# Kernel optimization log

Hardware: AMD Instinct MI355X
Metric: run time of the kernel (lower is better)

## Reference

```python
import jax, jax.numpy as jnp
import numpy as np

NUM_HEADS = 4

def setup_inputs() -> dict:
    key = jax.random.key(0)
    ks = jax.random.split(key, 9)
    C = 256
    def w(k, shape, scale):
        return jax.random.normal(k, shape, dtype=jnp.float32) * scale
    s = 1.0 / np.sqrt(C)
    return {
        'x':  w(ks[0], (1, C, 48, 48), 1.0),
        'Wq': w(ks[1], (C, C), s), 'bq': w(ks[2], (C,), 0.01),
        'Wk': w(ks[3], (C, C), s), 'bk': w(ks[4], (C,), 0.01),
        'Wv': w(ks[5], (C, C), s), 'bv': w(ks[6], (C,), 0.01),
        'Wo': w(ks[7], (C, C), s), 'bo': w(ks[8], (C,), 0.01),
    }

def reference(x, Wq, bq, Wk, bk, Wv, bv, Wo, bo):
    # x: [B, C, H, W] (NCHW like torch). 1x1 convs == per-pixel matmuls in NHWC.
    B, C, H, W = x.shape
    nh = NUM_HEADS
    xt = jnp.transpose(x, (0, 2, 3, 1))                 # [B,H,W,C]
    q = xt @ Wq.T + bq                                  # [B,H,W,Ck]
    k = xt @ Wk.T + bk                                  # [B,H,W,Ck]
    v = xt @ Wv.T + bv                                  # [B,H,W,Cv]
    dk = q.shape[-1] // nh
    dv = v.shape[-1] // nh
    # split heads then FULLY flatten (batch*H*W*heads), as in the original
    qf = q.reshape(B * H * W * nh, dk) / jnp.sqrt(jnp.float32(dk))
    kf = k.reshape(B * H * W * nh, dk)
    vf = v.reshape(B * H * W * nh, dv)
    A = jax.nn.softmax(qf @ kf.T, axis=1)               # [N,N], N = B*H*W*nh
    # dropout is identity in eval mode
    O = A @ vf                                          # [N,dv]
    O = O.reshape(B, H, W, nh * dv)                     # heads folded back into channels
    out = O @ Wo.T + bo                                 # 1x1 output conv
    return jnp.transpose(out, (0, 3, 1, 2))             # [B,Cout,H,W]
```

## Files before the change

### kernel.cpp

```cpp
#include <hip/hip_runtime.h>
#include <stdint.h>

typedef __attribute__((ext_vector_type(4))) float f32x4;
typedef __attribute__((ext_vector_type(8))) short bf16x8;

#define MFMA(a, b, c) __builtin_amdgcn_mfma_f32_16x16x32_bf16(a, b, c, 0, 0, 0)

__device__ __forceinline__ short f2b(float f) {
    uint32_t u = __builtin_bit_cast(uint32_t, f);
    u += 0x7fffu + ((u >> 16) & 1u);
    return (short)(u >> 16);
}

__device__ __forceinline__ float ex2(float x) {
    float r; asm("v_exp_f32 %0, %1" : "=v"(r) : "v"(x)); return r;
}
__device__ __forceinline__ float ex2c(float x) { return ex2(fminf(x, 60.0f)); }
__device__ __forceinline__ uint32_t cvtpk(float lo, float hi) {
    uint32_t r; asm("v_cvt_pk_bf16_f32 %0, %1, %2" : "=v"(r) : "v"(lo), "v"(hi)); return r;
}
__device__ __forceinline__ float lo2f(uint32_t u) {
    return __builtin_bit_cast(float, (uint32_t)(u << 16));
}
__device__ __forceinline__ float hi2f(uint32_t u) {
    return __builtin_bit_cast(float, (uint32_t)(u & 0xffff0000u));
}

typedef __attribute__((address_space(1))) const uint32_t gu32;
typedef __attribute__((address_space(3))) uint32_t su32;
__device__ __forceinline__ void stage16(const void* g, void* s) {
    __builtin_amdgcn_global_load_lds((gu32*)g, (su32*)s, 16, 0, 0);
}

__device__ __forceinline__ int FSW(int r) { return (r & 3) | (((r >> 3) & 1) << 2); }

#define QSCALE 0.1803368801111601f

__global__ __launch_bounds__(256) void kp_16(
    const float* __restrict__ x,
    const float* __restrict__ Wq, const float* __restrict__ Wk,
    const float* __restrict__ Wv, const float* __restrict__ Wo,
    short* __restrict__ Wall, short* __restrict__ xt) {
    __shared__ float tile[64][65];
    if (blockIdx.x < 1024) {
        int idx = blockIdx.x * 256 + threadIdx.x;
        int row = idx >> 8, col = idx & 255;
        float v;
        if (row < 256)      v = Wq[row * 256 + col];
        else if (row < 512) v = Wk[(row - 256) * 256 + col];
        else if (row < 768) v = Wv[(row - 512) * 256 + col];
        else                v = Wo[(row - 768) * 256 + col];
        Wall[idx] = f2b(v);
    } else {
        int b = blockIdx.x - 1024;
        int pbase = (b % 36) * 64, cbase = (b / 36) * 64;
        int tx = threadIdx.x & 63, tq = threadIdx.x >> 6;
        #pragma unroll
        for (int r = 0; r < 16; r++) {
            int row = tq * 16 + r;
            tile[row][tx] = x[(cbase + row) * 2304 + pbase + tx];
        }
        __syncthreads();
        #pragma unroll
        for (int r = 0; r < 16; r++) {
            int prow = tq * 16 + r;
            xt[(pbase + prow) * 256 + cbase + tx] = f2b(tile[tx][prow]);
        }
    }
}

__global__ __launch_bounds__(256) void kqkv_16(
    const short* __restrict__ Wall, const short* __restrict__ xt,
    const float* __restrict__ bq, const float* __restrict__ bk, const float* __restrict__ bv,
    short* __restrict__ Qf, short* __restrict__ Kf, short* __restrict__ Vt) {
    int t = threadIdx.x, wave = t >> 6, lane = t & 63, lr = lane & 15, lg = lane >> 4;
    int obase = blockIdx.x * 64 + wave * 16;
    int pbase = blockIdx.y * 64;
    const short* arow  = Wall + (obase + lr) * 256 + lg * 8;
    const short* brow0 = xt + (pbase +  0 + lr) * 256 + lg * 8;
    const short* brow1 = xt + (pbase + 16 + lr) * 256 + lg * 8;
    const short* brow2 = xt + (pbase + 32 + lr) * 256 + lg * 8;
    const short* brow3 = xt + (pbase + 48 + lr) * 256 + lg * 8;
    f32x4 acc0 = {0,0,0,0}, acc1 = {0,0,0,0}, acc2 = {0,0,0,0}, acc3 = {0,0,0,0};
    #pragma unroll
    for (int ks = 0; ks < 8; ks++) {
        bf16x8 a = *(const bf16x8*)(arow + ks * 32);
        acc0 = MFMA(a, *(const bf16x8*)(brow0 + ks * 32), acc0);
        acc1 = MFMA(a, *(const bf16x8*)(brow1 + ks * 32), acc1);
        acc2 = MFMA(a, *(const bf16x8*)(brow2 + ks * 32), acc2);
        acc3 = MFMA(a, *(const bf16x8*)(brow3 + ks * 32), acc3);
    }
    int w_idx = obase >> 8;
    const float* bias = (w_idx == 0) ? bq : (w_idx == 1) ? bk : bv;
    f32x4 accs[4] = {acc0, acc1, acc2, acc3};
    #pragma unroll
    for (int i = 0; i < 4; i++) {
        int o = obase + 4 * lg + i;
        int oo = o & 255;
        float b = bias[oo];
        int h = oo >> 6, d = oo & 63;
        #pragma unroll
        for (int ct = 0; ct < 4; ct++) {
            int p = pbase + ct * 16 + lr;
            float val = accs[ct][i] + b;
            int n = p * 4 + h;
            if (w_idx == 0)      Qf[n * 64 + d] = f2b(val * QSCALE);
            else if (w_idx == 1) Kf[n * 64 + d] = f2b(val);
            else                 Vt[d * 9216 + n] = f2b(val);
        }
    }
}

__global__ __launch_bounds__(256) void kat_16(
    const short* __restrict__ Qf, const short* __restrict__ Kf,
    const short* __restrict__ Vt, int keysPer, int ntiles,
    float* __restrict__ ps, uint32_t* __restrict__ pacc) {
    __shared__ short ktile[2][4096];
    __shared__ short vtile[2][4096];
    int t = threadIdx.x, wave = t >> 6, lane = t & 63, lr = lane & 15, lg = lane >> 4;
    int kb = blockIdx.y;
    int qbase = blockIdx.x * 128 + wave * 16;
    int kstart = kb * keysPer;

    const short* qrowA = Qf + (qbase + lr) * 64 + lg * 8;
    bf16x8 qA0 = *(const bf16x8*)(qrowA);
    bf16x8 qA1 = *(const bf16x8*)(qrowA + 32);
    const short* qrowB = qrowA + 64 * 64;
    bf16x8 qB0 = *(const bf16x8*)(qrowB);
    bf16x8 qB1 = *(const bf16x8*)(qrowB + 32);

    bf16x8 ones;
    #pragma unroll
    for (int i = 0; i < 8; i++) ones[i] = (short)0x3F80;

    int sr = lane >> 3, slot = lane & 7;
    int srow0 = wave * 16 + sr, srow1 = srow0 + 8;
    int col0 = (slot ^ FSW(srow0)) << 4;
    int col1 = (slot ^ FSW(srow1)) << 4;
    const char* kS0 = (const char*)Kf + (size_t)(kstart + srow0) * 128 + col0;
    const char* kS1 = (const char*)Kf + (size_t)(kstart + srow1) * 128 + col1;
    const char* vS0 = (const char*)Vt + (size_t)srow0 * 18432 + (size_t)kstart * 2 + col0;
    const char* vS1 = (const char*)Vt + (size_t)srow1 * 18432 + (size_t)kstart * 2 + col1;
    short* kD0[2] = { &ktile[0][wave * 1024], &ktile[1][wave * 1024] };
    short* kD1[2] = { kD0[0] + 512, kD0[1] + 512 };
    short* vD0[2] = { &vtile[0][wave * 1024], &vtile[1][wave * 1024] };
    short* vD1[2] = { vD0[0] + 512, vD0[1] + 512 };

    int perm = (lr & 3) + 8 * (lr >> 2);
    int cb = lg * 16;
    int kOffA0 = perm * 128       + (cb        ^ (FSW(perm) << 4));
    int kOffA1 = perm * 128       + ((cb + 64) ^ (FSW(perm) << 4));
    int kOffB0 = (perm + 4) * 128 + (cb        ^ (FSW(perm + 4) << 4));
    int kOffB1 = (perm + 4) * 128 + ((cb + 64) ^ (FSW(perm + 4) << 4));
    int vOff   = lr * 128         + (cb        ^ (FSW(lr) << 4));

    f32x4 zv = {0,0,0,0};
    f32x4 accA0 = zv, accA1 = zv, accA2 = zv, accA3 = zv, saccA = zv;
    f32x4 accB0 = zv, accB1 = zv, accB2 = zv, accB3 = zv, saccB = zv;

    stage16(kS0, kD0[0]); stage16(kS1, kD1[0]);
    stage16(vS0, vD0[0]); stage16(vS1, vD1[0]);

    for (int tt = 0; tt < ntiles; tt++) {
        __syncthreads();
        int buf = tt & 1;
        if (tt + 1 < ntiles) {
            size_t ko = (size_t)(tt + 1) * 8192, vo = (size_t)(tt + 1) * 128;
            stage16(kS0 + ko, kD0[buf ^ 1]); stage16(kS1 + ko, kD1[buf ^ 1]);
            stage16(vS0 + vo, vD0[buf ^ 1]); stage16(vS1 + vo, vD1[buf ^ 1]);
        }
        const char* kt = (const char*)&ktile[buf][0];
        const char* vt = (const char*)&vtile[buf][0];

        bf16x8 kA0 = *(const bf16x8*)(kt + kOffA0);
        bf16x8 kA1 = *(const bf16x8*)(kt + kOffA1);
        bf16x8 kB0 = *(const bf16x8*)(kt + kOffB0);
        bf16x8 kB1 = *(const bf16x8*)(kt + kOffB1);
        f32x4 sA0 = MFMA(kA0, qA0, zv); sA0 = MFMA(kA1, qA1, sA0);
        f32x4 sA1 = MFMA(kB0, qA0, zv); sA1 = MFMA(kB1, qA1, sA1);
        f32x4 sB0 = MFMA(kA0, qB0, zv); sB0 = MFMA(kA1, qB1, sB0);
        f32x4 sB1 = MFMA(kB0, qB0, zv); sB1 = MFMA(kB1, qB1, sB1);
        kA0 = *(const bf16x8*)(kt + 4096 + kOffA0);
        kA1 = *(const bf16x8*)(kt + 4096 + kOffA1);
        kB0 = *(const bf16x8*)(kt + 4096 + kOffB0);
        kB1 = *(const bf16x8*)(kt + 4096 + kOffB1);
        f32x4 sA2 = MFMA(kA0, qA0, zv); sA2 = MFMA(kA1, qA1, sA2);
        f32x4 sA3 = MFMA(kB0, qA0, zv); sA3 = MFMA(kB1, qA1, sA3);
        f32x4 sB2 = MFMA(kA0, qB0, zv); sB2 = MFMA(kA1, qB1, sB2);
        f32x4 sB3 = MFMA(kB0, qB0, zv); sB3 = MFMA(kB1, qB1, sB3);

        union { uint32_t w[4]; bf16x8 v; } paA, pbA, paB, pbB;
        paA.w[0] = cvtpk(ex2c(sA0[0]), ex2c(sA0[1]));
        paA.w[1] = cvtpk(ex2c(sA0[2]), ex2c(sA0[3]));
        paA.w[2] = cvtpk(ex2c(sA1[0]), ex2c(sA1[1]));
        paA.w[3] = cvtpk(ex2c(sA1[2]), ex2c(sA1[3]));
        pbA.w[0] = cvtpk(ex2c(sA2[0]), ex2c(sA2[1]));
        pbA.w[1] = cvtpk(ex2c(sA2[2]), ex2c(sA2[3]));
        pbA.w[2] = cvtpk(ex2c(sA3[0]), ex2c(sA3[1]));
        pbA.w[3] = cvtpk(ex2c(sA3[2]), ex2c(sA3[3]));
        paB.w[0] = cvtpk(ex2c(sB0[0]), ex2c(sB0[1]));
        paB.w[1] = cvtpk(ex2c(sB0[2]), ex2c(sB0[3]));
        paB.w[2] = cvtpk(ex2c(sB1[0]), ex2c(sB1[1]));
        paB.w[3] = cvtpk(ex2c(sB1[2]), ex2c(sB1[3]));
        pbB.w[0] = cvtpk(ex2c(sB2[0]), ex2c(sB2[1]));
        pbB.w[1] = cvtpk(ex2c(sB2[2]), ex2c(sB2[3]));
        pbB.w[2] = cvtpk(ex2c(sB3[0]), ex2c(sB3[1]));
        pbB.w[3] = cvtpk(ex2c(sB3[2]), ex2c(sB3[3]));

        bf16x8 v0a = *(const bf16x8*)(vt + vOff);
        bf16x8 v0b = *(const bf16x8*)(vt + (vOff ^ 64));
        bf16x8 v1a = *(const bf16x8*)(vt + vOff + 2048);
        bf16x8 v1b = *(const bf16x8*)(vt + ((vOff + 2048) ^ 64));
        bf16x8 v2a = *(const bf16x8*)(vt + vOff + 4096);
        bf16x8 v2b = *(const bf16x8*)(vt + ((vOff + 4096) ^ 64));
        bf16x8 v3a = *(const bf16x8*)(vt + vOff + 6144);
        bf16x8 v3b = *(const bf16x8*)(vt + ((vOff + 6144) ^ 64));
        accA0 = MFMA(v0a, paA.v, accA0); accA0 = MFMA(v0b, pbA.v, accA0);
        accA1 = MFMA(v1a, paA.v, accA1); accA1 = MFMA(v1b, pbA.v, accA1);
        accA2 = MFMA(v2a, paA.v, accA2); accA2 = MFMA(v2b, pbA.v, accA2);
        accA3 = MFMA(v3a, paA.v, accA3); accA3 = MFMA(v3b, pbA.v, accA3);
        saccA = MFMA(ones, paA.v, saccA); saccA = MFMA(ones, pbA.v, saccA);
        accB0 = MFMA(v0a, paB.v, accB0); accB0 = MFMA(v0b, pbB.v, accB0);
        accB1 = MFMA(v1a, paB.v, accB1); accB1 = MFMA(v1b, pbB.v, accB1);
        accB2 = MFMA(v2a, paB.v, accB2); accB2 = MFMA(v2b, pbB.v, accB2);
        accB3 = MFMA(v3a, paB.v, accB3); accB3 = MFMA(v3b, pbB.v, accB3);
        saccB = MFMA(ones, paB.v, saccB); saccB = MFMA(ones, pbB.v, saccB);
    }

    int gA = blockIdx.x * 8 + wave;
    int gB = gA + 4;
    int pidxA = kb * 576 + gA, pidxB = kb * 576 + gB;
    uint2* outA = (uint2*)pacc + (size_t)pidxA * 256 + lr * 16 + lg;
    uint2* outB = (uint2*)pacc + (size_t)pidxB * 256 + lr * 16 + lg;
    uint2 w;
    w.x = cvtpk(accA0[0], accA0[1]); w.y = cvtpk(accA0[2], accA0[3]); outA[0]  = w;
    w.x = cvtpk(accA1[0], accA1[1]); w.y = cvtpk(accA1[2], accA1[3]); outA[4]  = w;
    w.x = cvtpk(accA2[0], accA2[1]); w.y = cvtpk(accA2[2], accA2[3]); outA[8]  = w;
    w.x = cvtpk(accA3[0], accA3[1]); w.y = cvtpk(accA3[2], accA3[3]); outA[12] = w;
    w.x = cvtpk(accB0[0], accB0[1]); w.y = cvtpk(accB0[2], accB0[3]); outB[0]  = w;
    w.x = cvtpk(accB1[0], accB1[1]); w.y = cvtpk(accB1[2], accB1[3]); outB[4]  = w;
    w.x = cvtpk(accB2[0], accB2[1]); w.y = cvtpk(accB2[2], accB2[3]); outB[8]  = w;
    w.x = cvtpk(accB3[0], accB3[1]); w.y = cvtpk(accB3[2], accB3[3]); outB[12] = w;
    if (lg == 0) {
        ps[pidxA * 16 + lr] = saccA[0];
        ps[pidxB * 16 + lr] = saccB[0];
    }
}

__global__ __launch_bounds__(256) void kcmb_16(
    const float* __restrict__ ps, const uint32_t* __restrict__ pacc,
    short* __restrict__ Of, int nsplit) {
    int qb = blockIdx.x, t = threadIdx.x;
    int q = t >> 4, dv4 = (t & 15) * 4;
    float S = 0.f;
    f32x4 O = {0, 0, 0, 0};
    for (int s = 0; s < nsplit; s++) {
        S += ps[(s * 576 + qb) * 16 + q];
        uint2 v = ((const uint2*)pacc)[(size_t)(s * 576 + qb) * 256 + t];
        O[0] += lo2f(v.x); O[1] += hi2f(v.x);
        O[2] += lo2f(v.y); O[3] += hi2f(v.y);
    }
    float inv = 1.0f / fmaxf(S, 1e-30f);
    uint32_t w0 = cvtpk(O[0] * inv, O[1] * inv);
    uint32_t w1 = cvtpk(O[2] * inv, O[3] * inv);
    int n = qb * 16 + q, p = n >> 2, hh = n & 3;
    uint2 pk; pk.x = w0; pk.y = w1;
    *(uint2*)(&Of[p * 256 + hh * 64 + dv4]) = pk;
}

__global__ __launch_bounds__(256) void kout_16(
    const short* __restrict__ Wo_bf, const short* __restrict__ Of,
    const float* __restrict__ bo, float* __restrict__ out) {
    int t = threadIdx.x, wave = t >> 6, lane = t & 63, lr = lane & 15, lg = lane >> 4;
    int obase = blockIdx.x * 64 + wave * 16;
    int pbase = blockIdx.y * 64;
    const short* arow  = Wo_bf + (obase + lr) * 256 + lg * 8;
    const short* brow0 = Of + (pbase +  0 + lr) * 256 + lg * 8;
    const short* brow1 = Of + (pbase + 16 + lr) * 256 + lg * 8;
    const short* brow2 = Of + (pbase + 32 + lr) * 256 + lg * 8;
    const short* brow3 = Of + (pbase + 48 + lr) * 256 + lg * 8;
    f32x4 acc0 = {0,0,0,0}, acc1 = {0,0,0,0}, acc2 = {0,0,0,0}, acc3 = {0,0,0,0};
    #pragma unroll
    for (int ks = 0; ks < 8; ks++) {
        bf16x8 a = *(const bf16x8*)(arow + ks * 32);
        acc0 = MFMA(a, *(const bf16x8*)(brow0 + ks * 32), acc0);
        acc1 = MFMA(a, *(const bf16x8*)(brow1 + ks * 32), acc1);
        acc2 = MFMA(a, *(const bf16x8*)(brow2 + ks * 32), acc2);
        acc3 = MFMA(a, *(const bf16x8*)(brow3 + ks * 32), acc3);
    }
    f32x4 accs[4] = {acc0, acc1, acc2, acc3};
    #pragma unroll
    for (int i = 0; i < 4; i++) {
        int o = obase + 4 * lg + i;
        float b = bo[o];
        #pragma unroll
        for (int ct = 0; ct < 4; ct++) {
            int p = pbase + ct * 16 + lr;
            out[o * 2304 + p] = accs[ct][i] + b;
        }
    }
}

extern "C" void kernel_launch(void* const* d_in, const int* in_sizes, int n_in,
                              void* d_out, int out_size, void* d_ws, size_t ws_size,
                              hipStream_t stream) {
    const float* x  = (const float*)d_in[0];
    const float* Wq = (const float*)d_in[1];
    const float* bq = (const float*)d_in[2];
    const float* Wk = (const float*)d_in[3];
    const float* bk = (const float*)d_in[4];
    const float* Wv = (const float*)d_in[5];
    const float* bv = (const float*)d_in[6];
    const float* Wo = (const float*)d_in[7];
    const float* bo = (const float*)d_in[8];

    char* ws = (char*)d_ws;
    short* Wall = (short*)(ws);
    short* xt   = (short*)(ws + 524288);
    short* Qf   = (short*)(ws + 1703936);
    short* Kf   = (short*)(ws + 2883584);
    short* Vt   = (short*)(ws + 4063232);
    short* Of   = (short*)(ws + 5242880);
    float* ps   = (float*)(ws + 6422528);
    uint32_t* pacc = (uint32_t*)(ws + 7012352);
    float* out  = (float*)d_out;

    size_t base = 7012352;
    int nsplit = (ws_size >= base + 16u * 576u * 2048u) ? 16
               : (ws_size >= base +  8u * 576u * 2048u) ? 8 : 4;
    int keysPer = 9216 / nsplit;
    int ntiles = keysPer / 64;

    kp_16<<<1168, 256, 0, stream>>>(x, Wq, Wk, Wv, Wo, Wall, xt);
    kqkv_16<<<dim3(12, 36), 256, 0, stream>>>(Wall, xt, bq, bk, bv, Qf, Kf, Vt);
    kat_16<<<dim3(72, nsplit), 256, 0, stream>>>(Qf, Kf, Vt, keysPer, ntiles, ps, pacc);
    kcmb_16<<<576, 256, 0, stream>>>(ps, pacc, Of, nsplit);
    kout_16<<<dim3(4, 36), 256, 0, stream>>>(Wall + 768 * 256, Of, bo, out);
}
```

Baseline: 71.37 us.

## Halve attention queries per block and reduce key split count

The attention kernel now handles 64 queries per block (one 16-row group per wave) instead of 128, so each K/V tile staged in LDS is reused by half as many queries. The grid doubles along the query axis. The maximum key split drops from 16 to 8, which gives each block more key tiles and less partial data for the combine kernel to read. Register pressure falls and occupancy may rise, but K/V traffic from global memory into LDS doubles for each query.

Result: no change. 72.62 us (+1.8%).

```diff
diff --git a/kernel.cpp b/kernel.cpp
--- a/kernel.cpp
+++ b/kernel.cpp
@@ -36,7 +36,7 @@
 
 #define QSCALE 0.1803368801111601f
 
-__global__ __launch_bounds__(256) void kp_16(
+__global__ __launch_bounds__(256) void kp_17(
     const float* __restrict__ x,
     const float* __restrict__ Wq, const float* __restrict__ Wk,
     const float* __restrict__ Wv, const float* __restrict__ Wo,
@@ -69,7 +69,7 @@
     }
 }
 
-__global__ __launch_bounds__(256) void kqkv_16(
+__global__ __launch_bounds__(256) void kqkv_17(
     const short* __restrict__ Wall, const short* __restrict__ xt,
     const float* __restrict__ bq, const float* __restrict__ bk, const float* __restrict__ bv,
     short* __restrict__ Qf, short* __restrict__ Kf, short* __restrict__ Vt) {
@@ -111,7 +111,7 @@
     }
 }
 
-__global__ __launch_bounds__(256) void kat_16(
+__global__ __launch_bounds__(256) void kat_17(
     const short* __restrict__ Qf, const short* __restrict__ Kf,
     const short* __restrict__ Vt, int keysPer, int ntiles,
     float* __restrict__ ps, uint32_t* __restrict__ pacc) {
@@ -119,15 +119,12 @@
     __shared__ short vtile[2][4096];
     int t = threadIdx.x, wave = t >> 6, lane = t & 63, lr = lane & 15, lg = lane >> 4;
     int kb = blockIdx.y;
-    int qbase = blockIdx.x * 128 + wave * 16;
+    int qbase = blockIdx.x * 64 + wave * 16;
     int kstart = kb * keysPer;
 
-    const short* qrowA = Qf + (qbase + lr) * 64 + lg * 8;
-    bf16x8 qA0 = *(const bf16x8*)(qrowA);
-    bf16x8 qA1 = *(const bf16x8*)(qrowA + 32);
-    const short* qrowB = qrowA + 64 * 64;
-    bf16x8 qB0 = *(const bf16x8*)(qrowB);
-    bf16x8 qB1 = *(const bf16x8*)(qrowB + 32);
+    const short* qrow = Qf + (qbase + lr) * 64 + lg * 8;
+    bf16x8 q0 = *(const bf16x8*)(qrow);
+    bf16x8 q1 = *(const bf16x8*)(qrow + 32);
 
     bf16x8 ones;
     #pragma unroll
@@ -155,8 +152,7 @@
     int vOff   = lr * 128         + (cb        ^ (FSW(lr) << 4));
 
     f32x4 zv = {0,0,0,0};
-    f32x4 accA0 = zv, accA1 = zv, accA2 = zv, accA3 = zv, saccA = zv;
-    f32x4 accB0 = zv, accB1 = zv, accB2 = zv, accB3 = zv, saccB = zv;
+    f32x4 acc0 = zv, acc1 = zv, acc2 = zv, acc3 = zv, sacc = zv;
 
     stage16(kS0, kD0[0]); stage16(kS1, kD1[0]);
     stage16(vS0, vD0[0]); stage16(vS1, vD1[0]);
@@ -176,36 +172,24 @@
         bf16x8 kA1 = *(const bf16x8*)(kt + kOffA1);
         bf16x8 kB0 = *(const bf16x8*)(kt + kOffB0);
         bf16x8 kB1 = *(const bf16x8*)(kt + kOffB1);
-        f32x4 sA0 = MFMA(kA0, qA0, zv); sA0 = MFMA(kA1, qA1, sA0);
-        f32x4 sA1 = MFMA(kB0, qA0, zv); sA1 = MFMA(kB1, qA1, sA1);
-        f32x4 sB0 = MFMA(kA0, qB0, zv); sB0 = MFMA(kA1, qB1, sB0);
-        f32x4 sB1 = MFMA(kB0, qB0, zv); sB1 = MFMA(kB1, qB1, sB1);
+        f32x4 s0 = MFMA(kA0, q0, zv); s0 = MFMA(kA1, q1, s0);
+        f32x4 s1 = MFMA(kB0, q0, zv); s1 = MFMA(kB1, q1, s1);
         kA0 = *(const bf16x8*)(kt + 4096 + kOffA0);
         kA1 = *(const bf16x8*)(kt + 4096 + kOffA1);
         kB0 = *(const bf16x8*)(kt + 4096 + kOffB0);
         kB1 = *(const bf16x8*)(kt + 4096 + kOffB1);
-        f32x4 sA2 = MFMA(kA0, qA0, zv); sA2 = MFMA(kA1, qA1, sA2);
-        f32x4 sA3 = MFMA(kB0, qA0, zv); sA3 = MFMA(kB1, qA1, sA3);
-        f32x4 sB2 = MFMA(kA0, qB0, zv); sB2 = MFMA(kA1, qB1, sB2);
-        f32x4 sB3 = MFMA(kB0, qB0, zv); sB3 = MFMA(kB1, qB1, sB3);
-
-        union { uint32_t w[4]; bf16x8 v; } paA, pbA, paB, pbB;
-        paA.w[0] = cvtpk(ex2c(sA0[0]), ex2c(sA0[1]));
-        paA.w[1] = cvtpk(ex2c(sA0[2]), ex2c(sA0[3]));
-        paA.w[2] = cvtpk(ex2c(sA1[0]), ex2c(sA1[1]));
-        paA.w[3] = cvtpk(ex2c(sA1[2]), ex2c(sA1[3]));
-        pbA.w[0] = cvtpk(ex2c(sA2[0]), ex2c(sA2[1]));
-        pbA.w[1] = cvtpk(ex2c(sA2[2]), ex2c(sA2[3]));
-        pbA.w[2] = cvtpk(ex2c(sA3[0]), ex2c(sA3[1]));
-        pbA.w[3] = cvtpk(ex2c(sA3[2]), ex2c(sA3[3]));
-        paB.w[0] = cvtpk(ex2c(sB0[0]), ex2c(sB0[1]));
-        paB.w[1] = cvtpk(ex2c(sB0[2]), ex2c(sB0[3]));
-        paB.w[2] = cvtpk(ex2c(sB1[0]), ex2c(sB1[1]));
-        paB.w[3] = cvtpk(ex2c(sB1[2]), ex2c(sB1[3]));
-        pbB.w[0] = cvtpk(ex2c(sB2[0]), ex2c(sB2[1]));
-        pbB.w[1] = cvtpk(ex2c(sB2[2]), ex2c(sB2[3]));
-        pbB.w[2] = cvtpk(ex2c(sB3[0]), ex2c(sB3[1]));
-        pbB.w[3] = cvtpk(ex2c(sB3[2]), ex2c(sB3[3]));
+        f32x4 s2 = MFMA(kA0, q0, zv); s2 = MFMA(kA1, q1, s2);
+        f32x4 s3 = MFMA(kB0, q0, zv); s3 = MFMA(kB1, q1, s3);
+
+        union { uint32_t w[4]; bf16x8 v; } pa, pb;
+        pa.w[0] = cvtpk(ex2c(s0[0]), ex2c(s0[1]));
+        pa.w[1] = cvtpk(ex2c(s0[2]), ex2c(s0[3]));
+        pa.w[2] = cvtpk(ex2c(s1[0]), ex2c(s1[1]));
+        pa.w[3] = cvtpk(ex2c(s1[2]), ex2c(s1[3]));
+        pb.w[0] = cvtpk(ex2c(s2[0]), ex2c(s2[1]));
+        pb.w[1] = cvtpk(ex2c(s2[2]), ex2c(s2[3]));
+        pb.w[2] = cvtpk(ex2c(s3[0]), ex2c(s3[1]));
+        pb.w[3] = cvtpk(ex2c(s3[2]), ex2c(s3[3]));
 
         bf16x8 v0a = *(const bf16x8*)(vt + vOff);
         bf16x8 v0b = *(const bf16x8*)(vt + (vOff ^ 64));
@@ -215,39 +199,27 @@
         bf16x8 v2b = *(const bf16x8*)(vt + ((vOff + 4096) ^ 64));
         bf16x8 v3a = *(const bf16x8*)(vt + vOff + 6144);
         bf16x8 v3b = *(const bf16x8*)(vt + ((vOff + 6144) ^ 64));
-        accA0 = MFMA(v0a, paA.v, accA0); accA0 = MFMA(v0b, pbA.v, accA0);
-        accA1 = MFMA(v1a, paA.v, accA1); accA1 = MFMA(v1b, pbA.v, accA1);
-        accA2 = MFMA(v2a, paA.v, accA2); accA2 = MFMA(v2b, pbA.v, accA2);
-        accA3 = MFMA(v3a, paA.v, accA3); accA3 = MFMA(v3b, pbA.v, accA3);
-        saccA = MFMA(ones, paA.v, saccA); saccA = MFMA(ones, pbA.v, saccA);
-        accB0 = MFMA(v0a, paB.v, accB0); accB0 = MFMA(v0b, pbB.v, accB0);
-        accB1 = MFMA(v1a, paB.v, accB1); accB1 = MFMA(v1b, pbB.v, accB1);
-        accB2 = MFMA(v2a, paB.v, accB2); accB2 = MFMA(v2b, pbB.v, accB2);
-        accB3 = MFMA(v3a, paB.v, accB3); accB3 = MFMA(v3b, pbB.v, accB3);
-        saccB = MFMA(ones, paB.v, saccB); saccB = MFMA(ones, pbB.v, saccB);
-    }
-
-    int gA = blockIdx.x * 8 + wave;
-    int gB = gA + 4;
-    int pidxA = kb * 576 + gA, pidxB = kb * 576 + gB;
-    uint2* outA = (uint2*)pacc + (size_t)pidxA * 256 + lr * 16 + lg;
-    uint2* outB = (uint2*)pacc + (size_t)pidxB * 256 + lr * 16 + lg;
+        acc0 = MFMA(v0a, pa.v, acc0); acc0 = MFMA(v0b, pb.v, acc0);
+        acc1 = MFMA(v1a, pa.v, acc1); acc1 = MFMA(v1b, pb.v, acc1);
+        acc2 = MFMA(v2a, pa.v, acc2); acc2 = MFMA(v2b, pb.v, acc2);
+        acc3 = MFMA(v3a, pa.v, acc3); acc3 = MFMA(v3b, pb.v, acc3);
+        sacc = MFMA(ones, pa.v, sacc); sacc = MFMA(ones, pb.v, sacc);
+    }
+
+    int g = blockIdx.x * 4 + wave;
+    int pidx = kb * 576 + g;
+    uint2* outp = (uint2*)pacc + (size_t)pidx * 256 + lr * 16 + lg;
     uint2 w;
-    w.x = cvtpk(accA0[0], accA0[1]); w.y = cvtpk(accA0[2], accA0[3]); outA[0]  = w;
-    w.x = cvtpk(accA1[0], accA1[1]); w.y = cvtpk(accA1[2], accA1[3]); outA[4]  = w;
-    w.x = cvtpk(accA2[0], accA2[1]); w.y = cvtpk(accA2[2], accA2[3]); outA[8]  = w;
-    w.x = cvtpk(accA3[0], accA3[1]); w.y = cvtpk(accA3[2], accA3[3]); outA[12] = w;
-    w.x = cvtpk(accB0[0], accB0[1]); w.y = cvtpk(accB0[2], accB0[3]); outB[0]  = w;
-    w.x = cvtpk(accB1[0], accB1[1]); w.y = cvtpk(accB1[2], accB1[3]); outB[4]  = w;
-    w.x = cvtpk(accB2[0], accB2[1]); w.y = cvtpk(accB2[2], accB2[3]); outB[8]  = w;
-    w.x = cvtpk(accB3[0], accB3[1]); w.y = cvtpk(accB3[2], accB3[3]); outB[12] = w;
+    w.x = cvtpk(acc0[0], acc0[1]); w.y = cvtpk(acc0[2], acc0[3]); outp[0]  = w;
+    w.x = cvtpk(acc1[0], acc1[1]); w.y = cvtpk(acc1[2], acc1[3]); outp[4]  = w;
+    w.x = cvtpk(acc2[0], acc2[1]); w.y = cvtpk(acc2[2], acc2[3]); outp[8]  = w;
+    w.x = cvtpk(acc3[0], acc3[1]); w.y = cvtpk(acc3[2], acc3[3]); outp[12] = w;
     if (lg == 0) {
-        ps[pidxA * 16 + lr] = saccA[0];
-        ps[pidxB * 16 + lr] = saccB[0];
-    }
-}
-
-__global__ __launch_bounds__(256) void kcmb_16(
+        ps[pidx * 16 + lr] = sacc[0];
+    }
+}
+
+__global__ __launch_bounds__(256) void kcmb_17(
     const float* __restrict__ ps, const uint32_t* __restrict__ pacc,
     short* __restrict__ Of, int nsplit) {
     int qb = blockIdx.x, t = threadIdx.x;
@@ -268,7 +240,7 @@
     *(uint2*)(&Of[p * 256 + hh * 64 + dv4]) = pk;
 }
 
-__global__ __launch_bounds__(256) void kout_16(
+__global__ __launch_bounds__(256) void kout_17(
     const short* __restrict__ Wo_bf, const short* __restrict__ Of,
     const float* __restrict__ bo, float* __restrict__ out) {
     int t = threadIdx.x, wave = t >> 6, lane = t & 63, lr = lane & 15, lg = lane >> 4;
@@ -326,14 +298,13 @@
     float* out  = (float*)d_out;
 
     size_t base = 7012352;
-    int nsplit = (ws_size >= base + 16u * 576u * 2048u) ? 16
-               : (ws_size >= base +  8u * 576u * 2048u) ? 8 : 4;
+    int nsplit = (ws_size >= base + 8u * 576u * 2048u) ? 8 : 4;
     int keysPer = 9216 / nsplit;
     int ntiles = keysPer / 64;
 
-    kp_16<<<1168, 256, 0, stream>>>(x, Wq, Wk, Wv, Wo, Wall, xt);
-    kqkv_16<<<dim3(12, 36), 256, 0, stream>>>(Wall, xt, bq, bk, bv, Qf, Kf, Vt);
-    kat_16<<<dim3(72, nsplit), 256, 0, stream>>>(Qf, Kf, Vt, keysPer, ntiles, ps, pacc);
-    kcmb_16<<<576, 256, 0, stream>>>(ps, pacc, Of, nsplit);
-    kout_16<<<dim3(4, 36), 256, 0, stream>>>(Wall + 768 * 256, Of, bo, out);
-}
+    kp_17<<<1168, 256, 0, stream>>>(x, Wq, Wk, Wv, Wo, Wall, xt);
+    kqkv_17<<<dim3(12, 36), 256, 0, stream>>>(Wall, xt, bq, bk, bv, Qf, Kf, Vt);
+    kat_17<<<dim3(144, nsplit), 256, 0, stream>>>(Qf, Kf, Vt, keysPer, ntiles, ps, pacc);
+    kcmb_17<<<576, 256, 0, stream>>>(ps, pacc, Of, nsplit);
+    kout_17<<<dim3(4, 36), 256, 0, stream>>>(Wall + 768 * 256, Of, bo, out);
+}
```
